# Kernel tuning notes

Hardware: AMD Instinct MI355X
Metric: run time of the kernel (lower is better)

The kernel has to match this reference:

```python
import jax, jax.numpy as jnp
import numpy as np

DIM = 1024
HEADS = 16
DIM_HEAD = 64
NUM_FREQS = 16
INNER = HEADS * DIM_HEAD


def rotate_half(x):
    # matches torch: cat((-x[..., 1::2], x[..., ::2]), dim=-1)
    x1 = x[..., ::2]
    x2 = x[..., 1::2]
    return jnp.concatenate((-x2, x1), axis=-1)


def rope_fourier_cache(seq_len, head_dim, num_freqs):
    freqs = 10000.0 ** (-jnp.arange(0, head_dim, 2, dtype=jnp.float32) / head_dim)  # [hd/2]
    pos = jnp.arange(seq_len, dtype=jnp.float32)[:, None]  # [n,1]
    angles = pos * freqs  # [n, hd/2]
    sin = jnp.sin(angles)
    cos = jnp.cos(angles)
    # interleave-duplicate each value per pair: [n, hd]
    sin = jnp.stack([sin, sin], axis=-1).reshape(seq_len, head_dim)
    cos = jnp.stack([cos, cos], axis=-1).reshape(seq_len, head_dim)
    ffreqs = jnp.arange(1, num_freqs + 1, dtype=jnp.float32)  # [F]
    p = jnp.arange(seq_len, dtype=jnp.float32)[:, None]  # [n,1]
    fourier = jnp.concatenate([jnp.sin(p * ffreqs), jnp.cos(p * ffreqs)], axis=-1)  # [n, 2F]
    return sin, cos, fourier


def setup_inputs() -> dict:
    key = jax.random.key(0)
    ks = jax.random.split(key, 6)
    b, n = 4, 2048
    x = jax.random.normal(ks[0], (b, n, DIM), dtype=jnp.float32)
    w_qkv = jax.random.normal(ks[1], (3 * INNER, DIM), dtype=jnp.float32) * (DIM ** -0.5)
    w_fproj = jax.random.normal(ks[2], (DIM_HEAD, 2 * NUM_FREQS), dtype=jnp.float32) * ((2 * NUM_FREQS) ** -0.5)
    b_fproj = jax.random.normal(ks[3], (DIM_HEAD,), dtype=jnp.float32) * 0.02
    w_out = jax.random.normal(ks[4], (DIM, INNER), dtype=jnp.float32) * (INNER ** -0.5)
    b_out = jax.random.normal(ks[5], (DIM,), dtype=jnp.float32) * 0.02
    return {"x": x, "w_qkv": w_qkv, "w_fproj": w_fproj, "b_fproj": b_fproj,
            "w_out": w_out, "b_out": b_out}


def reference(x, w_qkv, w_fproj, b_fproj, w_out, b_out):
    b, n, _ = x.shape
    scale = DIM_HEAD ** -0.5
    qkv = x @ w_qkv.T  # [b, n, 3*inner]
    q, k, v = jnp.split(qkv, 3, axis=-1)
    def to_heads(t):
        return t.reshape(b, n, HEADS, DIM_HEAD).transpose(0, 2, 1, 3)  # [b,h,n,d]
    q, k, v = to_heads(q), to_heads(k), to_heads(v)
    sin, cos, fourier = rope_fourier_cache(n, DIM_HEAD, NUM_FREQS)
    fenc = fourier @ w_fproj.T + b_fproj  # [n, d]
    fenc = fenc[None, None]  # [1,1,n,d]
    q = q * cos + rotate_half(q) * sin + fenc
    k = k * cos + rotate_half(k) * sin + fenc
    dots = jnp.einsum('bhid,bhjd->bhij', q, k) * scale
    attn = jax.nn.softmax(dots, axis=-1)
    out = jnp.einsum('bhij,bhjd->bhid', attn, v)
    out = out.transpose(0, 2, 1, 3).reshape(b, n, INNER)
    return out @ w_out.T + b_out
```

## Files before the change

### kernel.cpp

```cpp
#include <hip/hip_runtime.h>
#include <math.h>

#define NB 4
#define SEQ 2048
#define DIMM 1024
#define NH 16
#define DHD 64
#define NFQ 16

typedef __bf16 bf16x8 __attribute__((ext_vector_type(8)));
typedef __bf16 bf16x4 __attribute__((ext_vector_type(4)));
typedef float f32x4 __attribute__((ext_vector_type(4)));

#if __has_builtin(__builtin_amdgcn_exp2f)
#define EXP2F(x) __builtin_amdgcn_exp2f(x)
#else
#define EXP2F(x) exp2f(x)
#endif

__device__ inline unsigned short f2bf(float f) {
  unsigned int u = __builtin_bit_cast(unsigned int, f);
  u += 0x7fffu + ((u >> 16) & 1u);
  return (unsigned short)(u >> 16);
}

#define GLL16(gp, lp) __builtin_amdgcn_global_load_lds( \
    (__attribute__((address_space(1))) void*)(gp), \
    (__attribute__((address_space(3))) void*)(lp), 16, 0, 0)

__global__ __launch_bounds__(64) void rope_tab_kernel(const float* __restrict__ w_fproj,
                                                      const float* __restrict__ b_fproj,
                                                      float4* __restrict__ tab) {
  const int pos = blockIdx.x;
  const int d = threadIdx.x;
  __shared__ float four[2 * NFQ];
  if (d < NFQ) {
    double a = (double)pos * (double)(d + 1);
    four[d] = (float)sin(a);
    four[d + NFQ] = (float)cos(a);
  }
  __syncthreads();
  float fe = b_fproj[d];
  const float* wr = w_fproj + d * 2 * NFQ;
#pragma unroll
  for (int j = 0; j < 2 * NFQ; ++j) fe += four[j] * wr[j];
  const int i = d >> 1;
  const double freq = exp(((double)(-2 * i)) / 64.0 * log(10000.0));
  const float angle = (float)pos * (float)freq;
  const float c = (float)cos((double)angle);
  const float s = (float)sin((double)angle);
  tab[(pos << 6) + d] = make_float4(c, s, fe, 0.f);
}

__global__ __launch_bounds__(256) void f2bf_kernel(const float* __restrict__ src,
                                                   unsigned short* __restrict__ dst, int n4) {
  for (int i = blockIdx.x * 256 + threadIdx.x; i < n4; i += gridDim.x * 256) {
    const float4 v = ((const float4*)src)[i];
    ushort4 o;
    o.x = f2bf(v.x); o.y = f2bf(v.y); o.z = f2bf(v.z); o.w = f2bf(v.w);
    ((ushort4*)dst)[i] = o;
  }
}

template<int EPI>
__global__ __launch_bounds__(256) void gemm_bt(const unsigned short* __restrict__ A,
                                               const unsigned short* __restrict__ Bw,
                                               int K,
                                               float* __restrict__ outF,
                                               unsigned short* __restrict__ outQ,
                                               unsigned short* __restrict__ outK,
                                               unsigned short* __restrict__ outV,
                                               const float4* __restrict__ tab,
                                               const float* __restrict__ bias,
                                               float qscale) {
  __shared__ __align__(16) unsigned short As[2][128 * 32];
  __shared__ __align__(16) unsigned short Bs[2][128 * 32];
  const int t = threadIdx.x, l = t & 63, w = t >> 6;
  const int wr = w >> 1, wc = w & 1;
  const int orig = blockIdx.x + gridDim.x * blockIdx.y;
  const int xcd = orig & 7, idx = orig >> 3;
  const int sc = idx >> 5, r5 = idx & 31;
  const int bm = ((xcd << 3) + (r5 >> 2)) * 128;
  const int bn = ((sc << 2) + (r5 & 3)) * 128;
  const f32x4 z = {0.f, 0.f, 0.f, 0.f};
  f32x4 acc[4][4];
#pragma unroll
  for (int m = 0; m < 4; ++m)
#pragma unroll
    for (int n = 0; n < 4; ++n) acc[m][n] = z;

  auto stage = [&](int k0, int buf) {
#pragma unroll
    for (int j = 0; j < 2; ++j) {
      const int Bb = w * 2048 + j * 1024 + l * 16;
      const int row = Bb >> 6, bin = Bb & 63;
      const int sb = bin ^ ((row & 3) << 4);
      GLL16(A  + (size_t)(bm + row) * K + k0 + (sb >> 1), (char*)(&As[buf][0]) + w * 2048 + j * 1024);
      GLL16(Bw + (size_t)(bn + row) * K + k0 + (sb >> 1), (char*)(&Bs[buf][0]) + w * 2048 + j * 1024);
    }
  };

  stage(0, 0);
  stage(32, 1);
  for (int k0 = 0; k0 < K; k0 += 32) {
    const int cur = (k0 >> 5) & 1;
    if (k0 + 32 < K) asm volatile("s_waitcnt vmcnt(4)" ::: "memory");
    else             asm volatile("s_waitcnt vmcnt(0)" ::: "memory");
    __builtin_amdgcn_s_barrier();

    bf16x8 af[4], bfr[4];
#pragma unroll
    for (int m = 0; m < 4; ++m) {
      const int row = wr * 64 + m * 16 + (l & 15);
      const int bin = ((l >> 4) * 16) ^ ((row & 3) << 4);
      af[m] = *(const bf16x8*)((const char*)(&As[cur][0]) + row * 64 + bin);
    }
#pragma unroll
    for (int n = 0; n < 4; ++n) {
      const int row = wc * 64 + n * 16 + (l & 15);
      const int bin = ((l >> 4) * 16) ^ ((row & 3) << 4);
      bfr[n] = *(const bf16x8*)((const char*)(&Bs[cur][0]) + row * 64 + bin);
    }
#pragma unroll
    for (int m = 0; m < 4; ++m)
#pragma unroll
      for (int n = 0; n < 4; ++n)
        acc[m][n] = __builtin_amdgcn_mfma_f32_16x16x32_bf16(af[m], bfr[n], acc[m][n], 0, 0, 0);

    asm volatile("s_waitcnt lgkmcnt(0)" ::: "memory");
    __builtin_amdgcn_s_barrier();
    if (k0 + 64 < K) stage(k0 + 64, cur);
  }

  const int c = l & 15;
  if (EPI == 0) {
    const int which = bn >> 10;
    const int h = ((bn & 1023) >> 6) + wc;
    if (which == 2) {
#pragma unroll
      for (int m = 0; m < 4; ++m)
#pragma unroll
        for (int n = 0; n < 4; ++n) {
          const int d = n * 16 + c;
#pragma unroll
          for (int r = 0; r < 4; ++r) {
            const int mrow = bm + wr * 64 + m * 16 + (l >> 4) * 4 + r;
            const int b = mrow >> 11, pos = mrow & (SEQ - 1);
            outV[((size_t)(b * NH + h) * DHD + d) * SEQ + pos] = f2bf(acc[m][n][r]);
          }
        }
    } else {
      unsigned short* dst = (which == 0) ? outQ : outK;
      const float sc2 = (which == 0) ? qscale : 1.f;
      const int laneE = (l & 48) | ((2 * c) & 15);
      const int laneO = (l & 48) | ((2 * c + 1) & 15);
      const bool hi = (c >= 8);
#pragma unroll
      for (int m = 0; m < 4; ++m)
#pragma unroll
        for (int r = 0; r < 4; ++r) {
          const int mrow = bm + wr * 64 + m * 16 + (l >> 4) * 4 + r;
          const int b = mrow >> 11, pos = mrow & (SEQ - 1);
          const float V0 = acc[m][0][r], V1 = acc[m][1][r];
          const float V2 = acc[m][2][r], V3 = acc[m][3][r];
          const float e0 = __shfl(V0, laneE), e1 = __shfl(V1, laneE);
          const float e2 = __shfl(V2, laneE), e3 = __shfl(V3, laneE);
          const float o0 = __shfl(V0, laneO), o1 = __shfl(V1, laneO);
          const float o2 = __shfl(V2, laneO), o3 = __shfl(V3, laneO);
          const float rot0 = -(hi ? o1 : o0);
          const float rot1 = -(hi ? o3 : o2);
          const float rot2 =  (hi ? e1 : e0);
          const float rot3 =  (hi ? e3 : e2);
          const float4 t0 = tab[(pos << 6) + c];
          const float4 t1 = tab[(pos << 6) + 16 + c];
          const float4 t2 = tab[(pos << 6) + 32 + c];
          const float4 t3 = tab[(pos << 6) + 48 + c];
          unsigned short* drow = dst + ((size_t)(b * NH + h) * SEQ + pos) * DHD + c;
          drow[0]  = f2bf((V0 * t0.x + rot0 * t0.y + t0.z) * sc2);
          drow[16] = f2bf((V1 * t1.x + rot1 * t1.y + t1.z) * sc2);
          drow[32] = f2bf((V2 * t2.x + rot2 * t2.y + t2.z) * sc2);
          drow[48] = f2bf((V3 * t3.x + rot3 * t3.y + t3.z) * sc2);
        }
    }
  } else {
#pragma unroll
    for (int m = 0; m < 4; ++m)
#pragma unroll
      for (int n = 0; n < 4; ++n) {
        const int ncol = bn + wc * 64 + n * 16 + c;
        const float bb = bias[ncol];
#pragma unroll
        for (int r = 0; r < 4; ++r) {
          const int mrow = bm + wr * 64 + m * 16 + (l >> 4) * 4 + r;
          outF[(size_t)mrow * DIMM + ncol] = acc[m][n][r] + bb;
        }
      }
  }
}

__global__ __launch_bounds__(256, 2) void attn_kernel(const unsigned short* __restrict__ qbf,
                                                      const unsigned short* __restrict__ kbf,
                                                      const unsigned short* __restrict__ vt,
                                                      unsigned short* __restrict__ ao) {
  __shared__ __align__(16) unsigned short Ks[2][64 * 64], Vts[2][64 * 64];
  __shared__ __align__(16) unsigned short Ps[4][64 * 64];
  const int t = threadIdx.x, l = t & 63, w = t >> 6, g = l >> 4, q = l & 15;
  int flat = blockIdx.x + (blockIdx.y << 3);
  flat = (flat & 7) * 64 + (flat >> 3);
  const int q0 = (flat & 7) * 256;
  const int bh = flat >> 3;
  const int b = bh >> 4, h = bh & 15;
  const size_t hbase = (size_t)bh * SEQ * DHD;
  const f32x4 z = {0.f, 0.f, 0.f, 0.f};
  const int swz = (q & 7) << 4;
  const int woff = w * 64;

  bf16x8 ones;
#pragma unroll
  for (int j = 0; j < 8; ++j) ones[j] = (__bf16)1.0f;

  auto stageKV = [&](int kt, int buf) {
#pragma unroll
    for (int j = 0; j < 2; ++j) {
      const int base = (w * 2 + j) * 1024;
      const int row = (base + l * 16) >> 7;
      const int sb = ((l & 7) * 16) ^ ((row & 7) << 4);
      GLL16(kbf + hbase + (size_t)(kt + row) * DHD + (sb >> 1),
            (char*)(&Ks[buf][0]) + base);
      GLL16(vt  + hbase + (size_t)row * SEQ + kt + (sb >> 1),
            (char*)(&Vts[buf][0]) + base);
    }
  };

  bf16x8 qf[4][2];
#pragma unroll
  for (int qb = 0; qb < 4; ++qb)
#pragma unroll
    for (int ks = 0; ks < 2; ++ks)
      qf[qb][ks] = *(const bf16x8*)(qbf + hbase +
          (size_t)(q0 + woff + qb * 16 + q) * DHD + ks * 32 + g * 8);

  stageKV(0, 0);
  stageKV(64, 1);

  f32x4 of[4][4], lsum[4];
#pragma unroll
  for (int qb = 0; qb < 4; ++qb) {
    lsum[qb] = z;
#pragma unroll
    for (int nd = 0; nd < 4; ++nd) of[qb][nd] = z;
  }

  for (int kt = 0; kt < SEQ; kt += 64) {
    const int cur = (kt >> 6) & 1;
    if (kt + 64 < SEQ) asm volatile("s_waitcnt vmcnt(4)" ::: "memory");
    else               asm volatile("s_waitcnt vmcnt(0)" ::: "memory");
    __builtin_amdgcn_s_barrier();

    const char* Kc = (const char*)(&Ks[cur][0]);
    const char* Vc = (const char*)(&Vts[cur][0]);

    f32x4 sf[4][4];
#pragma unroll
    for (int qb = 0; qb < 4; ++qb)
#pragma unroll
      for (int n = 0; n < 4; ++n) sf[qb][n] = z;
#pragma unroll
    for (int ks = 0; ks < 2; ++ks) {
      bf16x8 kf[4];
#pragma unroll
      for (int n = 0; n < 4; ++n)
        kf[n] = *(const bf16x8*)(Kc + (n * 16 + q) * 128 + ((ks * 64 + g * 16) ^ swz));
      __builtin_amdgcn_s_setprio(1);
#pragma unroll
      for (int qb = 0; qb < 4; ++qb)
#pragma unroll
        for (int n = 0; n < 4; ++n)
          sf[qb][n] = __builtin_amdgcn_mfma_f32_16x16x32_bf16(kf[n], qf[qb][ks], sf[qb][n], 0, 0, 0);
      __builtin_amdgcn_s_setprio(0);
    }

#pragma unroll
    for (int qb = 0; qb < 4; ++qb) {
      char* prow = (char*)(&Ps[w][0]) + (qb * 16 + q) * 128;
#pragma unroll
      for (int n = 0; n < 4; ++n) {
        bf16x4 pk;
        pk[0] = (__bf16)EXP2F(sf[qb][n][0]);
        pk[1] = (__bf16)EXP2F(sf[qb][n][1]);
        pk[2] = (__bf16)EXP2F(sf[qb][n][2]);
        pk[3] = (__bf16)EXP2F(sf[qb][n][3]);
        *(bf16x4*)(prow + ((n * 32 + g * 8) ^ swz)) = pk;
      }
    }

    bf16x8 vf[4][2];
#pragma unroll
    for (int nd = 0; nd < 4; ++nd)
#pragma unroll
      for (int ks = 0; ks < 2; ++ks)
        vf[nd][ks] = *(const bf16x8*)(Vc + (nd * 16 + q) * 128 + ((ks * 64 + g * 16) ^ swz));

#pragma unroll
    for (int qb = 0; qb < 4; ++qb) {
      const char* prow = (const char*)(&Ps[w][0]) + (qb * 16 + q) * 128;
      bf16x8 pa[2];
#pragma unroll
      for (int ks = 0; ks < 2; ++ks)
        pa[ks] = *(const bf16x8*)(prow + ((ks * 64 + g * 16) ^ swz));
      __builtin_amdgcn_s_setprio(1);
#pragma unroll
      for (int ks = 0; ks < 2; ++ks)
        lsum[qb] = __builtin_amdgcn_mfma_f32_16x16x32_bf16(pa[ks], ones, lsum[qb], 0, 0, 0);
#pragma unroll
      for (int nd = 0; nd < 4; ++nd)
#pragma unroll
        for (int ks = 0; ks < 2; ++ks)
          of[qb][nd] = __builtin_amdgcn_mfma_f32_16x16x32_bf16(pa[ks], vf[nd][ks], of[qb][nd], 0, 0, 0);
      __builtin_amdgcn_s_setprio(0);
    }

    asm volatile("s_waitcnt lgkmcnt(0)" ::: "memory");
    __builtin_amdgcn_s_barrier();
    if (kt + 128 < SEQ) stageKV(kt + 128, cur);
  }

#pragma unroll
  for (int qb = 0; qb < 4; ++qb)
#pragma unroll
    for (int r = 0; r < 4; ++r) {
      const float ir = 1.f / lsum[qb][r];
      const int pos = q0 + woff + qb * 16 + g * 4 + r;
#pragma unroll
      for (int nd = 0; nd < 4; ++nd) {
        const int col = h * DHD + nd * 16 + q;
        ao[((size_t)(b * SEQ + pos)) * DIMM + col] = f2bf(of[qb][nd][r] * ir);
      }
    }
}

extern "C" void kernel_launch(void* const* d_in, const int* in_sizes, int n_in,
                              void* d_out, int out_size, void* d_ws, size_t ws_size,
                              hipStream_t stream) {
  const float* x       = (const float*)d_in[0];
  const float* w_qkv   = (const float*)d_in[1];
  const float* w_fproj = (const float*)d_in[2];
  const float* b_fproj = (const float*)d_in[3];
  const float* w_out   = (const float*)d_in[4];
  const float* b_out   = (const float*)d_in[5];
  char* ws = (char*)d_ws;

  unsigned short* qbf    = (unsigned short*)(ws);
  unsigned short* kbf    = (unsigned short*)(ws + 16777216);
  unsigned short* vt     = (unsigned short*)(ws + 33554432);
  unsigned short* xbf    = (unsigned short*)(ws + 50331648);
  unsigned short* aobf   = (unsigned short*)(ws + 67108864);
  unsigned short* wqkvbf = (unsigned short*)(ws + 83886080);
  unsigned short* woutbf = (unsigned short*)(ws + 90177536);
  float4*         tab    = (float4*)(ws + 92274688);

  const float kLog2e = 1.4426950408889634f;

  hipLaunchKernelGGL(rope_tab_kernel, dim3(SEQ), dim3(DHD), 0, stream, w_fproj, b_fproj, tab);
  hipLaunchKernelGGL(f2bf_kernel, dim3(2048), dim3(256), 0, stream, x, xbf, (NB*SEQ*DIMM)/4);
  hipLaunchKernelGGL(f2bf_kernel, dim3(768), dim3(256), 0, stream, w_qkv, wqkvbf, (3*DIMM*DIMM)/4);
  hipLaunchKernelGGL(f2bf_kernel, dim3(256), dim3(256), 0, stream, w_out, woutbf, (DIMM*DIMM)/4);
  hipLaunchKernelGGL((gemm_bt<0>), dim3(24, 64), dim3(256), 0, stream,
                     xbf, wqkvbf, DIMM, (float*)nullptr, qbf, kbf, vt, tab,
                     (const float*)nullptr, 0.125f * kLog2e);
  hipLaunchKernelGGL(attn_kernel, dim3(SEQ/256, NB*NH), dim3(256), 0, stream, qbf, kbf, vt, aobf);
  hipLaunchKernelGGL((gemm_bt<1>), dim3(8, 64), dim3(256), 0, stream,
                     aobf, woutbf, DIMM, (float*)d_out, (unsigned short*)nullptr,
                     (unsigned short*)nullptr, (unsigned short*)nullptr, (const float4*)nullptr,
                     b_out, 1.0f);
}
```

Baseline: 191.9 us.

## Use 32x32 MFMA in attention with register-resident P and triple-buffer GEMM

```diff
diff --git a/kernel.cpp b/kernel.cpp
--- a/kernel.cpp
+++ b/kernel.cpp
@@ -11,6 +11,8 @@
 typedef __bf16 bf16x8 __attribute__((ext_vector_type(8)));
 typedef __bf16 bf16x4 __attribute__((ext_vector_type(4)));
 typedef float f32x4 __attribute__((ext_vector_type(4)));
+typedef float f32x16 __attribute__((ext_vector_type(16)));
+typedef unsigned int u32x4 __attribute__((ext_vector_type(4)));
 
 #if __has_builtin(__builtin_amdgcn_exp2f)
 #define EXP2F(x) __builtin_amdgcn_exp2f(x)
@@ -73,8 +75,8 @@
                                                const float4* __restrict__ tab,
                                                const float* __restrict__ bias,
                                                float qscale) {
-  __shared__ __align__(16) unsigned short As[2][128 * 32];
-  __shared__ __align__(16) unsigned short Bs[2][128 * 32];
+  __shared__ __align__(16) unsigned short As[3][128 * 32];
+  __shared__ __align__(16) unsigned short Bs[3][128 * 32];
   const int t = threadIdx.x, l = t & 63, w = t >> 6;
   const int wr = w >> 1, wc = w & 1;
   const int orig = blockIdx.x + gridDim.x * blockIdx.y;
@@ -100,12 +102,16 @@
     }
   };
 
+  const int NT = K >> 5;
   stage(0, 0);
-  stage(32, 1);
-  for (int k0 = 0; k0 < K; k0 += 32) {
-    const int cur = (k0 >> 5) & 1;
-    if (k0 + 32 < K) asm volatile("s_waitcnt vmcnt(4)" ::: "memory");
-    else             asm volatile("s_waitcnt vmcnt(0)" ::: "memory");
+  if (NT > 1) stage(32, 1);
+  if (NT > 2) stage(64, 2);
+  int cur = 0;
+  for (int it = 0; it < NT; ++it) {
+    const int rem = NT - 1 - it;
+    if (rem >= 2)      asm volatile("s_waitcnt vmcnt(8)" ::: "memory");
+    else if (rem == 1) asm volatile("s_waitcnt vmcnt(4)" ::: "memory");
+    else               asm volatile("s_waitcnt vmcnt(0)" ::: "memory");
     __builtin_amdgcn_s_barrier();
 
     bf16x8 af[4], bfr[4];
@@ -129,7 +135,8 @@
 
     asm volatile("s_waitcnt lgkmcnt(0)" ::: "memory");
     __builtin_amdgcn_s_barrier();
-    if (k0 + 64 < K) stage(k0 + 64, cur);
+    if (it + 3 < NT) stage((it + 3) * 32, cur);
+    cur = (cur == 2) ? 0 : cur + 1;
   }
 
   const int c = l & 15;
@@ -203,21 +210,16 @@
                                                       const unsigned short* __restrict__ vt,
                                                       unsigned short* __restrict__ ao) {
   __shared__ __align__(16) unsigned short Ks[2][64 * 64], Vts[2][64 * 64];
-  __shared__ __align__(16) unsigned short Ps[4][64 * 64];
-  const int t = threadIdx.x, l = t & 63, w = t >> 6, g = l >> 4, q = l & 15;
+  __shared__ float ltab[4][64];
+  const int t = threadIdx.x, l = t & 63, w = t >> 6;
+  const int G = l >> 5, c32 = l & 31;
   int flat = blockIdx.x + (blockIdx.y << 3);
   flat = (flat & 7) * 64 + (flat >> 3);
   const int q0 = (flat & 7) * 256;
   const int bh = flat >> 3;
   const int b = bh >> 4, h = bh & 15;
   const size_t hbase = (size_t)bh * SEQ * DHD;
-  const f32x4 z = {0.f, 0.f, 0.f, 0.f};
-  const int swz = (q & 7) << 4;
   const int woff = w * 64;
-
-  bf16x8 ones;
-#pragma unroll
-  for (int j = 0; j < 8; ++j) ones[j] = (__bf16)1.0f;
 
   auto stageKV = [&](int kt, int buf) {
 #pragma unroll
@@ -232,24 +234,25 @@
     }
   };
 
-  bf16x8 qf[4][2];
-#pragma unroll
-  for (int qb = 0; qb < 4; ++qb)
-#pragma unroll
-    for (int ks = 0; ks < 2; ++ks)
-      qf[qb][ks] = *(const bf16x8*)(qbf + hbase +
-          (size_t)(q0 + woff + qb * 16 + q) * DHD + ks * 32 + g * 8);
+  bf16x8 qf[2][4];
+#pragma unroll
+  for (int qg = 0; qg < 2; ++qg)
+#pragma unroll
+    for (int j = 0; j < 4; ++j)
+      qf[qg][j] = *(const bf16x8*)(qbf + hbase +
+          (size_t)(q0 + woff + qg * 32 + c32) * DHD + 16 * j + 8 * G);
 
   stageKV(0, 0);
   stageKV(64, 1);
 
-  f32x4 of[4][4], lsum[4];
-#pragma unroll
-  for (int qb = 0; qb < 4; ++qb) {
-    lsum[qb] = z;
-#pragma unroll
-    for (int nd = 0; nd < 4; ++nd) of[qb][nd] = z;
-  }
+  f32x16 of[2][2];
+  float psum[2] = {0.f, 0.f};
+#pragma unroll
+  for (int qg = 0; qg < 2; ++qg)
+#pragma unroll
+    for (int dg = 0; dg < 2; ++dg)
+#pragma unroll
+      for (int r = 0; r < 16; ++r) of[qg][dg][r] = 0.f;
 
   for (int kt = 0; kt < SEQ; kt += 64) {
     const int cur = (kt >> 6) & 1;
@@ -260,63 +263,68 @@
     const char* Kc = (const char*)(&Ks[cur][0]);
     const char* Vc = (const char*)(&Vts[cur][0]);
 
-    f32x4 sf[4][4];
-#pragma unroll
-    for (int qb = 0; qb < 4; ++qb)
-#pragma unroll
-      for (int n = 0; n < 4; ++n) sf[qb][n] = z;
-#pragma unroll
-    for (int ks = 0; ks < 2; ++ks) {
-      bf16x8 kf[4];
-#pragma unroll
-      for (int n = 0; n < 4; ++n)
-        kf[n] = *(const bf16x8*)(Kc + (n * 16 + q) * 128 + ((ks * 64 + g * 16) ^ swz));
+#pragma unroll
+    for (int ksub = 0; ksub < 2; ++ksub) {
+      f32x16 sf0, sf1;
+#pragma unroll
+      for (int r = 0; r < 16; ++r) { sf0[r] = 0.f; sf1[r] = 0.f; }
+      const int krow = ksub * 32 + c32;
+      const int kswz = (krow & 7) << 4;
       __builtin_amdgcn_s_setprio(1);
 #pragma unroll
-      for (int qb = 0; qb < 4; ++qb)
-#pragma unroll
-        for (int n = 0; n < 4; ++n)
-          sf[qb][n] = __builtin_amdgcn_mfma_f32_16x16x32_bf16(kf[n], qf[qb][ks], sf[qb][n], 0, 0, 0);
+      for (int j = 0; j < 4; ++j) {
+        const bf16x8 kf = *(const bf16x8*)(Kc + krow * 128 + ((32 * j + 16 * G) ^ kswz));
+        sf0 = __builtin_amdgcn_mfma_f32_32x32x16_bf16(kf, qf[0][j], sf0, 0, 0, 0);
+        sf1 = __builtin_amdgcn_mfma_f32_32x32x16_bf16(kf, qf[1][j], sf1, 0, 0, 0);
+      }
       __builtin_amdgcn_s_setprio(0);
-    }
-
-#pragma unroll
-    for (int qb = 0; qb < 4; ++qb) {
-      char* prow = (char*)(&Ps[w][0]) + (qb * 16 + q) * 128;
-#pragma unroll
-      for (int n = 0; n < 4; ++n) {
-        bf16x4 pk;
-        pk[0] = (__bf16)EXP2F(sf[qb][n][0]);
-        pk[1] = (__bf16)EXP2F(sf[qb][n][1]);
-        pk[2] = (__bf16)EXP2F(sf[qb][n][2]);
-        pk[3] = (__bf16)EXP2F(sf[qb][n][3]);
-        *(bf16x4*)(prow + ((n * 32 + g * 8) ^ swz)) = pk;
-      }
-    }
-
-    bf16x8 vf[4][2];
-#pragma unroll
-    for (int nd = 0; nd < 4; ++nd)
-#pragma unroll
-      for (int ks = 0; ks < 2; ++ks)
-        vf[nd][ks] = *(const bf16x8*)(Vc + (nd * 16 + q) * 128 + ((ks * 64 + g * 16) ^ swz));
-
-#pragma unroll
-    for (int qb = 0; qb < 4; ++qb) {
-      const char* prow = (const char*)(&Ps[w][0]) + (qb * 16 + q) * 128;
-      bf16x8 pa[2];
-#pragma unroll
-      for (int ks = 0; ks < 2; ++ks)
-        pa[ks] = *(const bf16x8*)(prow + ((ks * 64 + g * 16) ^ swz));
+
+      bf16x8 pa[2][2];
+#pragma unroll
+      for (int qg = 0; qg < 2; ++qg) {
+        const f32x16 sv = qg ? sf1 : sf0;
+        float p[16];
+#pragma unroll
+        for (int r = 0; r < 16; ++r) p[r] = EXP2F(sv[r]);
+        float s0 = 0.f;
+#pragma unroll
+        for (int r = 0; r < 16; ++r) s0 += p[r];
+        psum[qg] += s0;
+        unsigned W[8];
+#pragma unroll
+        for (int a = 0; a < 4; ++a)
+#pragma unroll
+          for (int hh = 0; hh < 2; ++hh)
+            asm("v_cvt_pk_bf16_f32 %0, %1, %2"
+                : "=v"(W[a * 2 + hh]) : "v"(p[4 * a + 2 * hh]), "v"(p[4 * a + 2 * hh + 1]));
+#pragma unroll
+        for (int m = 0; m < 2; ++m) {
+          const unsigned sendA = G ? W[4 * m + 0] : W[4 * m + 2];
+          const unsigned sendB = G ? W[4 * m + 1] : W[4 * m + 3];
+          const unsigned rA = (unsigned)__shfl_xor((int)sendA, 32);
+          const unsigned rB = (unsigned)__shfl_xor((int)sendB, 32);
+          const unsigned w0 = G ? rA : W[4 * m + 0];
+          const unsigned w1 = G ? rB : W[4 * m + 1];
+          const unsigned w2 = G ? W[4 * m + 2] : rA;
+          const unsigned w3 = G ? W[4 * m + 3] : rB;
+          const u32x4 tmp = {w0, w1, w2, w3};
+          pa[qg][m] = __builtin_bit_cast(bf16x8, tmp);
+        }
+      }
+
+      const int vrow0 = c32, vrow1 = 32 + c32;
+      const int vswz0 = (vrow0 & 7) << 4, vswz1 = (vrow1 & 7) << 4;
       __builtin_amdgcn_s_setprio(1);
 #pragma unroll
-      for (int ks = 0; ks < 2; ++ks)
-        lsum[qb] = __builtin_amdgcn_mfma_f32_16x16x32_bf16(pa[ks], ones, lsum[qb], 0, 0, 0);
-#pragma unroll
-      for (int nd = 0; nd < 4; ++nd)
-#pragma unroll
-        for (int ks = 0; ks < 2; ++ks)
-          of[qb][nd] = __builtin_amdgcn_mfma_f32_16x16x32_bf16(pa[ks], vf[nd][ks], of[qb][nd], 0, 0, 0);
+      for (int m = 0; m < 2; ++m) {
+        const int vb = 64 * ksub + 32 * m + 16 * G;
+        const bf16x8 vf0 = *(const bf16x8*)(Vc + vrow0 * 128 + (vb ^ vswz0));
+        const bf16x8 vf1 = *(const bf16x8*)(Vc + vrow1 * 128 + (vb ^ vswz1));
+        of[0][0] = __builtin_amdgcn_mfma_f32_32x32x16_bf16(pa[0][m], vf0, of[0][0], 0, 0, 0);
+        of[1][0] = __builtin_amdgcn_mfma_f32_32x32x16_bf16(pa[1][m], vf0, of[1][0], 0, 0, 0);
+        of[0][1] = __builtin_amdgcn_mfma_f32_32x32x16_bf16(pa[0][m], vf1, of[0][1], 0, 0, 0);
+        of[1][1] = __builtin_amdgcn_mfma_f32_32x32x16_bf16(pa[1][m], vf1, of[1][1], 0, 0, 0);
+      }
       __builtin_amdgcn_s_setprio(0);
     }
 
@@ -326,17 +334,25 @@
   }
 
 #pragma unroll
-  for (int qb = 0; qb < 4; ++qb)
-#pragma unroll
-    for (int r = 0; r < 4; ++r) {
-      const float ir = 1.f / lsum[qb][r];
-      const int pos = q0 + woff + qb * 16 + g * 4 + r;
-#pragma unroll
-      for (int nd = 0; nd < 4; ++nd) {
-        const int col = h * DHD + nd * 16 + q;
-        ao[((size_t)(b * SEQ + pos)) * DIMM + col] = f2bf(of[qb][nd][r] * ir);
-      }
-    }
+  for (int qg = 0; qg < 2; ++qg) {
+    const float tot = psum[qg] + __shfl_xor(psum[qg], 32);
+    if (l < 32) ltab[w][qg * 32 + c32] = tot;
+  }
+
+#pragma unroll
+  for (int qg = 0; qg < 2; ++qg) {
+#pragma unroll
+    for (int r = 0; r < 16; ++r) {
+      const int qrow = (r & 3) + 8 * (r >> 2) + 4 * G;
+      const float inv = 1.f / ltab[w][qg * 32 + qrow];
+      const int pos = q0 + woff + qg * 32 + qrow;
+#pragma unroll
+      for (int dg = 0; dg < 2; ++dg) {
+        const int col = h * DHD + dg * 32 + c32;
+        ao[((size_t)(b * SEQ + pos)) * DIMM + col] = f2bf(of[qg][dg][r] * inv);
+      }
+    }
+  }
 }
 
 extern "C" void kernel_launch(void* const* d_in, const int* in_sizes, int n_in,
```

New measurement: 196.8 us. 1.03x slower.
